# Kernel tuning notes

Hardware: AMD Instinct MI355X
Metric: run time of the kernel (lower is better)

The kernel has to match this reference:

```python
import jax, jax.numpy as jnp
import numpy as np

T, B, N = 12, 2, 1024
M = B * N            # nodes per timestep (batch-flattened)
D_IN, D_H, D_T, D_O = 64, 128, 16, 32


def _linear_params(k, fin, fout):
    kw, kb = jax.random.split(k)
    s = 1.0 / np.sqrt(fin)
    w = jax.random.uniform(kw, (fin, fout), jnp.float32, -s, s)
    b = jax.random.uniform(kb, (fout,), jnp.float32, -s, s)
    return w, b


def setup_inputs() -> dict:
    key = jax.random.key(0)
    ks = jax.random.split(key, 12)
    x = jax.random.normal(ks[0], (T, M, D_IN), jnp.float32)
    A = (jax.random.uniform(ks[1], (T, M, M)) < 0.01).astype(jnp.float32)
    A = A * (1.0 - jnp.eye(M, dtype=jnp.float32))  # no self-loops in raw adjacency
    ego_mask = jax.random.randint(ks[2], (B, T, N), 0, 2).astype(bool)
    gcn1_w, gcn1_b = _linear_params(ks[3], D_IN, D_H)
    gcn2_w, gcn2_b = _linear_params(ks[4], D_H, D_H)
    time_w, time_b = _linear_params(ks[5], 1, D_T)
    q_w, q_b = _linear_params(ks[6], D_H + D_T, D_H)
    k_w, k_b = _linear_params(ks[7], D_H + D_T, D_H)
    v_w, v_b = _linear_params(ks[8], D_H + D_T, D_H)
    o_w, o_b = _linear_params(ks[9], D_H, D_H)
    fc_w, fc_b = _linear_params(ks[10], D_H, D_O)
    return dict(x=x, A=A, ego_mask=ego_mask,
                gcn1_w=gcn1_w, gcn1_b=gcn1_b, gcn2_w=gcn2_w, gcn2_b=gcn2_b,
                time_w=time_w, time_b=time_b,
                q_w=q_w, q_b=q_b, k_w=k_w, k_b=k_b, v_w=v_w, v_b=v_b,
                o_w=o_w, o_b=o_b, fc_w=fc_w, fc_b=fc_b)


def _forward(x, A, ego_mask, gcn1_w, gcn1_b, gcn2_w, gcn2_b, time_w, time_b,
             q_w, q_b, k_w, k_b, v_w, v_b, o_w, o_b, fc_w, fc_b):
    # [B,T,N] -> [T, B*N], as in mask.permute(1,0,2).reshape(T,-1)
    mask = ego_mask.transpose(1, 0, 2).reshape(T, M)
    tvals = jnp.arange(T, dtype=jnp.float32)

    def step(_, inp):
        xt, At, mt, tv = inp  # [M,D_IN], [M,M], [M] bool, scalar
        m = mt.astype(xt.dtype)
        # restrict adjacency to masked subgraph; GCNConv adds self-loops
        A_hat = At * (m[:, None] * m[None, :]) + jnp.diag(m)
        deg = A_hat.sum(axis=0)  # in-degree per target (PyG gcn_norm on col)
        nrm = jnp.where(deg > 0, 1.0 / jnp.sqrt(jnp.maximum(deg, 1e-12)), 0.0)

        def gcn(h, w, b):
            # out[i] = nrm[i] * sum_j A_hat[j,i] * nrm[j] * (hW)[j] + b
            return (A_hat.T @ ((h @ w) * nrm[:, None])) * nrm[:, None] + b

        h = jax.nn.relu(gcn(xt, gcn1_w, gcn1_b))
        h = jax.nn.relu(gcn(h, gcn2_w, gcn2_b))
        # t_vec = sin(Linear(1,D_T)(t)) -- identical for all nodes
        t_vec = jnp.sin(tv * time_w[0] + time_b)  # [D_T]
        xtc = jnp.concatenate([h, jnp.broadcast_to(t_vec, (M, D_T))], axis=-1)
        Q = xtc @ q_w + q_b
        K = xtc @ k_w + k_b
        V = xtc @ v_w + v_b
        scores = (Q @ K.T) * (1.0 / np.sqrt(D_H))  # [M,M]
        scores = jnp.where(mt[None, :], scores, -1e9)  # keys restricted to mask
        agg = jax.nn.softmax(scores, axis=-1) @ V
        out = ((agg @ o_w + o_b) @ fc_w + fc_b) * m[:, None]  # scatter-back == mask
        return None, out

    _, outs = jax.lax.scan(step, None, (x, A, mask, tvals))  # [T,M,D_O]
    return outs.reshape(T, B, N, D_O).transpose(1, 2, 0, 3)  # [B,N,T,D_O]


def reference(x, A, ego_mask, gcn1_w, gcn1_b, gcn2_w, gcn2_b, time_w, time_b,
              q_w, q_b, k_w, k_b, v_w, v_b, o_w, o_b, fc_w, fc_b):
    return _forward(x, A, ego_mask, gcn1_w, gcn1_b, gcn2_w, gcn2_b, time_w,
                    time_b, q_w, q_b, k_w, k_b, v_w, v_b, o_w, o_b, fc_w, fc_b)
```

## Files before the change

kernel.cpp:

```cpp
#include <hip/hip_runtime.h>
#include <stdint.h>

#define TT   12
#define BB   2
#define NN   1024
#define MM   2048
#define TM   24576
#define DIN  64
#define DH   128
#define DOUT 32
#define CAP  64
#define OUTSZ 786432

typedef __attribute__((ext_vector_type(8))) short short8;
typedef __attribute__((ext_vector_type(4))) short short4v;
typedef __attribute__((ext_vector_type(4))) float f32x4;

#define MFMA(a,b,c) __builtin_amdgcn_mfma_f32_16x16x32_bf16((a),(b),(c),0,0,0)

__device__ __forceinline__ float bf2f(unsigned short u){
  union { uint32_t i; float f; } x; x.i = ((uint32_t)u) << 16; return x.f;
}
__device__ __forceinline__ unsigned short f2bf(float f){
  union { float f; uint32_t i; } x; x.f = f;
  uint32_t u = x.i + 0x7FFFu + ((x.i >> 16) & 1u);
  return (unsigned short)(u >> 16);
}
__device__ __forceinline__ float LD(const void* p, size_t i, int mode){
  return mode ? ((const float*)p)[i] : bf2f(((const unsigned short*)p)[i]);
}
__device__ __forceinline__ short8 ldx8(const void* x, size_t off, int md){
  if(md){
    const float4* xf = (const float4*)((const float*)x + off);
    float4 a = xf[0], b = xf[1];
    short8 o;
    o[0]=(short)f2bf(a.x); o[1]=(short)f2bf(a.y); o[2]=(short)f2bf(a.z); o[3]=(short)f2bf(a.w);
    o[4]=(short)f2bf(b.x); o[5]=(short)f2bf(b.y); o[6]=(short)f2bf(b.z); o[7]=(short)f2bf(b.w);
    return o;
  }
  return *(const short8*)((const unsigned short*)x + off);
}

__global__ void k_fill(float* __restrict__ out, int n, float val){
  int i = blockIdx.x*blockDim.x + threadIdx.x;
  if(i < n) out[i] = val;
}

__global__ void k_detect2(const unsigned short* __restrict__ x,
                          const unsigned char* __restrict__ eg,
                          int* __restrict__ dtf, int* __restrict__ flag,
                          int* __restrict__ nact){
  if(blockIdx.x == 0){
    __shared__ int cnt_s;
    if(threadIdx.x==0) cnt_s = 0;
    if(threadIdx.x < TT) nact[threadIdx.x] = 0;
    __syncthreads();
    int c = 0;
    for(int i=threadIdx.x; i<6144; i+=blockDim.x){
      unsigned short h = x[i*2];
      unsigned e = (h >> 7) & 0xFF;
      if(h==0 || (e >= 0x60 && e <= 0x9F)) c++;
    }
    atomicAdd(&cnt_s, c);
    __syncthreads();
    if(threadIdx.x==0) *dtf = (cnt_s > 4000) ? 0 : 1;
  } else {
    __shared__ int pres_s, ge2_s;
    if(threadIdx.x==0){ pres_s=0; ge2_s=0; }
    __syncthreads();
    int pres=0, ge2=0;
    for(int i=threadIdx.x; i<24576; i+=blockDim.x){
      unsigned v = eg[i];
      if(v){ pres |= 1 << (i & 7); if(v >= 2u) ge2 = 1; }
    }
    if(pres) atomicOr(&pres_s, pres);
    if(ge2)  atomicOr(&ge2_s, 1);
    __syncthreads();
    if(threadIdx.x==0){
      int pr = pres_s, g2 = ge2_s, mode;
      if(!g2){
        if((pr & ~0x01) == 0)      mode = 4;
        else if((pr & ~0x11) == 0) mode = 0;
        else                       mode = 1;
      } else {
        if((pr & ~0xC0) == 0)      mode = 5;
        else if((pr & ~0xCC) == 0) mode = 3;
        else                       mode = 2;
      }
      *flag = mode;
    }
  }
}

__global__ void k_mask(const void* __restrict__ egom, const int* __restrict__ flag,
                       int* __restrict__ cnt, int* __restrict__ nact,
                       int* __restrict__ aidx, int* __restrict__ inv,
                       float* __restrict__ out){
  int idx = blockIdx.x*blockDim.x + threadIdx.x;
  out[idx] = 0.f;
  if(idx >= TM) return;
  int t = idx / MM, node = idx % MM;
  int b = node / NN, n = node % NN;
  int src = (b*TT + t)*NN + n;
  int mode = *flag;
  int v;
  if(mode==0)      v = ((const int*)egom)[src] != 0;
  else if(mode==1) v = ((const unsigned char*)egom)[src] != 0;
  else if(mode==2) v = ((const unsigned short*)egom)[src] != 0;
  else if(mode==3) v = ((const float*)egom)[src] != 0.f;
  else if(mode==4) v = ((const long long*)egom)[src] != 0;
  else             v = ((const double*)egom)[src] != 0.0;
  cnt[idx] = 0;
  unsigned long long bal = __ballot(v != 0);
  int lane = threadIdx.x & 63;
  int base = 0;
  if(lane == 0 && bal) base = atomicAdd(&nact[t], __popcll(bal));
  base = __shfl(base, 0, 64);
  int ic = -1;
  if(v){
    int pfx = __popcll(bal & ((1ULL << lane) - 1ULL));
    ic = base + pfx;
    aidx[(size_t)t*MM + ic] = node;
  }
  inv[idx] = ic;
}

__global__ void k_prepw(
  const void* __restrict__ w1, const void* __restrict__ w2,
  const void* __restrict__ qw, const void* __restrict__ kw, const void* __restrict__ vw,
  const void* __restrict__ qb0, const void* __restrict__ kb0, const void* __restrict__ vb0,
  const void* __restrict__ ow, const void* __restrict__ ob,
  const void* __restrict__ fw, const void* __restrict__ fb,
  const void* __restrict__ tw, const void* __restrict__ tb,
  const void* __restrict__ b1, const void* __restrict__ b2,
  const int* __restrict__ dtf,
  unsigned short* __restrict__ W1t, unsigned short* __restrict__ W2t,
  unsigned short* __restrict__ Wqt, unsigned short* __restrict__ Wkt,
  unsigned short* __restrict__ Wvt, unsigned short* __restrict__ Wct,
  float* __restrict__ qbf, float* __restrict__ kbf, float* __restrict__ vbf,
  float* __restrict__ bcf, float* __restrict__ b1f, float* __restrict__ b2f)
{
  const int md = *dtf;
  int id = blockIdx.x*blockDim.x + threadIdx.x;
  if(id < 8192){
    int n=id&127, k2=id>>7; W1t[n*64+k2]=f2bf(LD(w1,(size_t)k2*128+n,md)); return; }
  id -= 8192;
  if(id < 16384){ int n=id&127,k2=id>>7; W2t[n*128+k2]=f2bf(LD(w2,(size_t)k2*128+n,md)); return; }
  id -= 16384;
  if(id < 16384){ int n=id&127,k2=id>>7; Wqt[n*128+k2]=f2bf(LD(qw,(size_t)k2*128+n,md)); return; }
  id -= 16384;
  if(id < 16384){ int n=id&127,k2=id>>7; Wkt[n*128+k2]=f2bf(LD(kw,(size_t)k2*128+n,md)); return; }
  id -= 16384;
  if(id < 16384){ int n=id&127,k2=id>>7; Wvt[n*128+k2]=f2bf(LD(vw,(size_t)k2*128+n,md)); return; }
  id -= 16384;
  if(id < 4096){
    int oc=id&31, c=id>>5; float s=0.f;
    for(int r=0;r<128;r++) s += LD(ow,(size_t)c*128+r,md)*LD(fw,(size_t)r*32+oc,md);
    Wct[oc*128+c]=f2bf(s); return;
  }
  id -= 4096;
  if(id < 32){
    float s = LD(fb,id,md);
    for(int r=0;r<128;r++) s += LD(ob,r,md)*LD(fw,(size_t)r*32+id,md);
    bcf[id]=s; return;
  }
  id -= 32;
  if(id < 4608){
    int which = id/1536, rem=id%1536, t=rem/128, n=rem%128;
    const void* W  = which==0?qw:(which==1?kw:vw);
    const void* Bs = which==0?qb0:(which==1?kb0:vb0);
    float s = LD(Bs,n,md);
    for(int d=0;d<16;d++){
      float tv = sinf((float)t*LD(tw,d,md) + LD(tb,d,md));
      s += tv * LD(W,(size_t)(128+d)*128+n,md);
    }
    float* dst = which==0?qbf:(which==1?kbf:vbf);
    dst[t*128+n]=s; return;
  }
  id -= 4608;
  if(id < 256){
    if(id<128) b1f[id] = LD(b1,id,md);
    else       b2f[id-128] = LD(b2,id-128,md);
    return;
  }
}

__global__ __launch_bounds__(256) void k_edges(const void* __restrict__ A,
    const int* __restrict__ dtf, const int* __restrict__ inv,
    int* __restrict__ cnt, int* __restrict__ edges){
  int id = blockIdx.x*blockDim.x + threadIdx.x;
  int seg = id & 63; int row = id >> 6;
  int t = row / MM;
  int jc = inv[row];
  if(jc < 0) return;
  const int* invt = inv + (size_t)t*MM;
  int* cb = cnt + (size_t)t*MM;
  int* eb = edges + (size_t)t*MM*CAP;
  if(*dtf){
    const float4* p4 = (const float4*)((const float*)A + (size_t)row*MM + seg*32);
    #pragma unroll
    for(int u=0;u<8;u++){
      float4 v = p4[u];
      float wd[4]={v.x,v.y,v.z,v.w};
      #pragma unroll
      for(int q=0;q<4;q++){
        if(wd[q]!=0.f){
          int ibc = invt[seg*32 + u*4 + q];
          if(ibc >= 0){ int s=atomicAdd(&cb[ibc],1); if(s<CAP) eb[(size_t)ibc*CAP+s]=jc; }
        }
      }
    }
  } else {
    const uint4* p4 = (const uint4*)((const unsigned short*)A + (size_t)row*MM + seg*32);
    #pragma unroll
    for(int u=0;u<4;u++){
      uint4 v = p4[u];
      unsigned wd[4]={v.x,v.y,v.z,v.w};
      #pragma unroll
      for(int q=0;q<4;q++){
        int ib = seg*32 + u*8 + q*2;
        if(wd[q] & 0xFFFFu){
          int ibc = invt[ib];
          if(ibc >= 0){ int s=atomicAdd(&cb[ibc],1); if(s<CAP) eb[(size_t)ibc*CAP+s]=jc; }
        }
        if(wd[q] >> 16){
          int ibc = invt[ib+1];
          if(ibc >= 0){ int s=atomicAdd(&cb[ibc],1); if(s<CAP) eb[(size_t)ibc*CAP+s]=jc; }
        }
      }
    }
  }
}

__global__ __launch_bounds__(256) void k_gemm_x(const void* __restrict__ x,
    const int* __restrict__ dtf, const int* __restrict__ nact,
    const int* __restrict__ aidx, const unsigned short* __restrict__ Wt,
    float* __restrict__ g)
{
  const int tile = blockIdx.x*64;
  const int t = tile / MM, il = tile % MM;
  const int na = nact[t];
  if(il >= ((na+63)&~63)) return;
  const int md = *dtf;
  const int tid=threadIdx.x, wv=tid>>6, lane=tid&63, l15=lane&15, quad=lane>>4;
  const int r0 = tile + (wv>>1)*32;
  const int c0 = (wv&1)*64;
  short8 bf[2][4];
  #pragma unroll
  for(int kk=0;kk<2;kk++)
    #pragma unroll
    for(int nt=0;nt<4;nt++)
      bf[kk][nt] = *(const short8*)(Wt + (size_t)(c0+nt*16+l15)*DIN + kk*32 + quad*8);
  const int il0 = (r0 % MM) + l15, il1 = (r0 % MM) + 16 + l15;
  const int n0 = aidx[(size_t)t*MM + (il0 < na ? il0 : 0)];
  const int n1 = aidx[(size_t)t*MM + (il1 < na ? il1 : 0)];
  const size_t xb0 = ((size_t)t*MM + n0)*DIN;
  const size_t xb1 = ((size_t)t*MM + n1)*DIN;
  f32x4 z = {0.f,0.f,0.f,0.f};
  f32x4 acc[2][4];
  #pragma unroll
  for(int i=0;i<2;i++){ acc[i][0]=z; acc[i][1]=z; acc[i][2]=z; acc[i][3]=z; }
  #pragma unroll
  for(int kk=0;kk<2;kk++){
    short8 a0 = ldx8(x, xb0 + kk*32 + quad*8, md);
    short8 a1 = ldx8(x, xb1 + kk*32 + quad*8, md);
    #pragma unroll
    for(int nt=0;nt<4;nt++){
      acc[0][nt]=MFMA(a0,bf[kk][nt],acc[0][nt]);
      acc[1][nt]=MFMA(a1,bf[kk][nt],acc[1][nt]);
    }
  }
  #pragma unroll
  for(int mt=0;mt<2;mt++)
    #pragma unroll
    for(int nt=0;nt<4;nt++){
      int col = c0+nt*16+l15;
      #pragma unroll
      for(int r=0;r<4;r++){
        int row = r0 + mt*16 + quad*4 + r;
        g[(size_t)row*DH + col] = acc[mt][nt][r];
      }
    }
}

__global__ __launch_bounds__(256) void k_gemm_h(const unsigned short* __restrict__ X,
    const unsigned short* __restrict__ Wt, float* __restrict__ g,
    const int* __restrict__ nact)
{
  const int tile = blockIdx.x*64;
  const int t = tile / MM, il = tile % MM;
  const int na = nact[t];
  if(il >= ((na+63)&~63)) return;
  const int tid=threadIdx.x, wv=tid>>6, lane=tid&63, l15=lane&15, quad=lane>>4;
  const int r0 = tile + (wv>>1)*32;
  const int c0 = (wv&1)*64;
  short8 bf[4][4];
  #pragma unroll
  for(int kk=0;kk<4;kk++)
    #pragma unroll
    for(int nt=0;nt<4;nt++)
      bf[kk][nt] = *(const short8*)(Wt + (size_t)(c0+nt*16+l15)*DH + kk*32 + quad*8);
  f32x4 z = {0.f,0.f,0.f,0.f};
  f32x4 acc[2][4];
  #pragma unroll
  for(int i=0;i<2;i++){ acc[i][0]=z; acc[i][1]=z; acc[i][2]=z; acc[i][3]=z; }
  #pragma unroll
  for(int kk=0;kk<4;kk++){
    short8 a0 = *(const short8*)(X + (size_t)(r0+l15)*DH    + kk*32 + quad*8);
    short8 a1 = *(const short8*)(X + (size_t)(r0+16+l15)*DH + kk*32 + quad*8);
    #pragma unroll
    for(int nt=0;nt<4;nt++){
      acc[0][nt]=MFMA(a0,bf[kk][nt],acc[0][nt]);
      acc[1][nt]=MFMA(a1,bf[kk][nt],acc[1][nt]);
    }
  }
  #pragma unroll
  for(int mt=0;mt<2;mt++)
    #pragma unroll
    for(int nt=0;nt<4;nt++){
      int col = c0+nt*16+l15;
      #pragma unroll
      for(int r=0;r<4;r++){
        int row = r0 + mt*16 + quad*4 + r;
        g[(size_t)row*DH + col] = acc[mt][nt][r];
      }
    }
}

__global__ __launch_bounds__(256) void k_gather(const float* __restrict__ g,
    const int* __restrict__ edges, const int* __restrict__ cnt,
    const int* __restrict__ nact, const float* __restrict__ bias,
    unsigned short* __restrict__ h)
{
  int wv = threadIdx.x>>6, lane = threadIdx.x&63;
  int gi = blockIdx.x*4 + wv;
// ... 37 lines not shown
  const int tid=threadIdx.x, wv=tid>>6, lane=tid&63, l15=lane&15, quad=lane>>4;
  const int r0 = tile + (wv>>1)*32;
  const int c0 = (wv&1)*64;
  short8 bf[4][4];
  #pragma unroll
  for(int kk=0;kk<4;kk++)
    #pragma unroll
    for(int nt=0;nt<4;nt++)
      bf[kk][nt] = *(const short8*)(Wt + (size_t)(c0+nt*16+l15)*DH + kk*32 + quad*8);
  f32x4 z = {0.f,0.f,0.f,0.f};
  f32x4 acc[2][4];
  #pragma unroll
  for(int i=0;i<2;i++){ acc[i][0]=z; acc[i][1]=z; acc[i][2]=z; acc[i][3]=z; }
  #pragma unroll
  for(int kk=0;kk<4;kk++){
    short8 a0 = *(const short8*)(X + (size_t)(r0+l15)*DH    + kk*32 + quad*8);
    short8 a1 = *(const short8*)(X + (size_t)(r0+16+l15)*DH + kk*32 + quad*8);
    #pragma unroll
    for(int nt=0;nt<4;nt++){
      acc[0][nt]=MFMA(a0,bf[kk][nt],acc[0][nt]);
      acc[1][nt]=MFMA(a1,bf[kk][nt],acc[1][nt]);
    }
  }
  if(which < 2){
    unsigned short* o = which==0 ? Qo : Ko;
    #pragma unroll
    for(int mt=0;mt<2;mt++)
      #pragma unroll
      for(int nt=0;nt<4;nt++){
        int col = c0+nt*16+l15;
        float bb = bias[t*DH+col];
        #pragma unroll
        for(int r=0;r<4;r++){
          int row = r0 + mt*16 + quad*4 + r;
          o[(size_t)row*DH + col] = f2bf(acc[mt][nt][r] + bb);
        }
      }
  } else {
    #pragma unroll
    for(int mt=0;mt<2;mt++)
      #pragma unroll
      for(int nt=0;nt<4;nt++){
        int col = c0+nt*16+l15;
        float bb = bias[t*DH+col];
        int node0 = il + (wv>>1)*32 + mt*16 + quad*4;
        short4v pk;
        #pragma unroll
        for(int r=0;r<4;r++) pk[r] = (short)f2bf(acc[mt][nt][r] + bb);
        *(short4v*)(Vtc + ((size_t)t*DH + col)*MM + node0) = pk;
      }
  }
}

__global__ __launch_bounds__(256) void k_attn(
  const unsigned short* __restrict__ Q, const unsigned short* __restrict__ Kc,
  const unsigned short* __restrict__ Vtc, const int* __restrict__ nact,
  const int* __restrict__ aidx, const unsigned short* __restrict__ Wct,
  const float* __restrict__ bc, float* __restrict__ out)
{
  __shared__ unsigned short Kl[64][136];
  __shared__ unsigned short Vl[128][72];
  __shared__ short Pl[4][16][72];
  __shared__ short Al[4][16][136];
  const int tid=threadIdx.x, wv=tid>>6, lane=tid&63, l15=lane&15, quad=lane>>4;
  const int t = blockIdx.y;
  const int na = nact[t];
  const int qblk = blockIdx.x*64;
  if(qblk >= na) return;
  const int qbase = qblk + wv*16;
  const float scale = 0.088388347648318447f;
  const int nkt = (na + 63) >> 6;

  short8 bq[4];
  #pragma unroll
  for(int kk=0;kk<4;kk++)
    bq[kk] = *(const short8*)(Q + ((size_t)t*MM + qbase + l15)*DH + kk*32 + quad*8);

  f32x4 zz = {0.f,0.f,0.f,0.f};
  f32x4 accPV[8];
  #pragma unroll
  for(int i=0;i<8;i++) accPV[i]=zz;
  float l_run = 0.f;

  const int srow = tid >> 2, sseg = tid & 3;
  const int vch  = tid >> 1, vhalf = tid & 1;

  short8 kreg[4], vreg[4];
  {
    const unsigned short* gk = Kc + ((size_t)t*MM + srow)*DH + sseg*32;
    const unsigned short* gv = Vtc + ((size_t)t*DH + vch)*MM + vhalf*32;
    #pragma unroll
    for(int j=0;j<4;j++){ kreg[j] = *(const short8*)(gk + j*8);
                          vreg[j] = *(const short8*)(gv + j*8); }
  }

  for(int kt=0; kt<nkt; kt++){
    const int key0 = kt*64;
    __syncthreads();
    {
      short8* kd = (short8*)&Kl[srow][sseg*32];
      short8* vd = (short8*)&Vl[vch][vhalf*32];
      #pragma unroll
      for(int j=0;j<4;j++){ kd[j] = kreg[j]; vd[j] = vreg[j]; }
    }
    __syncthreads();
    if(kt+1 < nkt){
      const int key1 = key0 + 64;
      const unsigned short* gk = Kc + ((size_t)t*MM + key1 + srow)*DH + sseg*32;
      const unsigned short* gv = Vtc + ((size_t)t*DH + vch)*MM + key1 + vhalf*32;
      #pragma unroll
      for(int j=0;j<4;j++){ kreg[j] = *(const short8*)(gk + j*8);
                            vreg[j] = *(const short8*)(gv + j*8); }
    }
    #pragma unroll
    for(int mt=0;mt<4;mt++){
      f32x4 s = zz;
      #pragma unroll
      for(int kk=0;kk<4;kk++){
        short8 ak = *(const short8*)&Kl[mt*16+l15][kk*32 + quad*8];
        s = MFMA(ak, bq[kk], s);
      }
      short4v pk;
      #pragma unroll
      for(int r=0;r<4;r++){
        float sv = fminf(fmaxf(s[r]*scale, -15.f), 15.f);
        float valid = (key0 + mt*16 + quad*4 + r < na) ? 1.f : 0.f;
        float p = __expf(sv) * valid;
        pk[r] = (short)f2bf(p);
        l_run += bf2f((unsigned short)pk[r]);
      }
      *(short4v*)&Pl[wv][l15][mt*16 + quad*4] = pk;
    }
    #pragma unroll
    for(int kk=0;kk<2;kk++){
      short8 ap = *(const short8*)&Pl[wv][l15][kk*32 + quad*8];
      #pragma unroll
      for(int nt=0;nt<8;nt++){
        short8 bv = *(const short8*)&Vl[nt*16+l15][kk*32 + quad*8];
        accPV[nt] = MFMA(ap, bv, accPV[nt]);
      }
    }
  }
  l_run += __shfl_xor(l_run, 16, 64);
  l_run += __shfl_xor(l_run, 32, 64);

  #pragma unroll
  for(int nt=0;nt<8;nt++)
    #pragma unroll
    for(int r=0;r<4;r++){
      float av = fminf(fmaxf(accPV[nt][r], -1e30f), 1e30f);
      Al[wv][quad*4+r][nt*16+l15] = (short)f2bf(av);
    }

  const int qc = qbase + l15;
  const bool qok = (qc < na);
  const float linv = (l_run > 0.f) ? 1.f/l_run : 0.f;
  const int node = aidx[(size_t)t*MM + (qok ? qc : 0)];
  #pragma unroll
  for(int mt2=0;mt2<2;mt2++){
    f32x4 d = zz;
    #pragma unroll
    for(int kk=0;kk<4;kk++){
      short8 aw = *(const short8*)(Wct + (size_t)(mt2*16+l15)*DH + kk*32 + quad*8);
      short8 bl = *(const short8*)&Al[wv][l15][kk*32 + quad*8];
      d = MFMA(aw, bl, d);
    }
    f32x4 bcv = *(const f32x4*)(bc + mt2*16 + quad*4);
    f32x4 o4;
    #pragma unroll
    for(int r=0;r<4;r++) o4[r] = d[r]*linv + bcv[r];
    if(qok)
      *(f32x4*)(out + (size_t)node*(TT*DOUT) + (size_t)t*DOUT + mt2*16 + quad*4) = o4;
  }
}

extern "C" void kernel_launch(void* const* d_in, const int* in_sizes, int n_in,
                              void* d_out, int out_size, void* d_ws, size_t ws_size,
                              hipStream_t stream)
{
  float* outp = (float*)d_out;
  static const int EXP[19] = {1572864,50331648,24576,8192,128,16384,128,16,16,
                              18432,128,18432,128,18432,128,16384,128,4096,32};
  bool ok = (n_in >= 19) && (out_size == OUTSZ);
  if(ok) for(int i=0;i<19;i++) if(in_sizes[i] != EXP[i]) { ok = false; break; }
  if(!ok){
    k_fill<<<(out_size+255)/256,256,0,stream>>>(outp, out_size, 1000.f);
    return;
  }
  const void* x   = d_in[0];
  const void* A   = d_in[1];
  const void* eg  = d_in[2];
  const void* w1  = d_in[3];
  const void* b1  = d_in[4];
  const void* w2  = d_in[5];
  const void* b2  = d_in[6];
  const void* tw  = d_in[7];
  const void* tb  = d_in[8];
  const void* qw  = d_in[9];
  const void* qb0 = d_in[10];
  const void* kw  = d_in[11];
  const void* kb0 = d_in[12];
  const void* vw  = d_in[13];
  const void* vb0 = d_in[14];
  const void* ow  = d_in[15];
  const void* ob  = d_in[16];
  const void* fw  = d_in[17];
  const void* fb  = d_in[18];

  char* w = (char*)d_ws;
  size_t off = 0;
  auto alloc = [&](size_t sz)->char*{
    char* p = w + off; off = (off + sz + 255) & ~(size_t)255; return p; };
  int*   flag  = (int*)  alloc(4);
  int*   dtf   = (int*)  alloc(4);
  int*   nactb = (int*)  alloc(TT*4);
  int*   cnt   = (int*)  alloc((size_t)TM*4);
  int*   aidx  = (int*)  alloc((size_t)TM*4);
  int*   inv   = (int*)  alloc((size_t)TM*4);
  int*   edges = (int*)  alloc((size_t)TM*CAP*4);
  float* g     = (float*)alloc((size_t)TM*DH*4);
  unsigned short* h   = (unsigned short*)alloc((size_t)TM*DH*2);
  unsigned short* Vtc = (unsigned short*)alloc((size_t)TT*DH*MM*2);
  unsigned short* W1t = (unsigned short*)alloc(DH*DIN*2);
  unsigned short* W2t = (unsigned short*)alloc(DH*DH*2);
  unsigned short* Wqt = (unsigned short*)alloc(DH*DH*2);
  unsigned short* Wkt = (unsigned short*)alloc(DH*DH*2);
  unsigned short* Wvt = (unsigned short*)alloc(DH*DH*2);
  unsigned short* Wct = (unsigned short*)alloc(DOUT*DH*2);
  float* qbf = (float*)alloc(TT*DH*4);
  float* kbf = (float*)alloc(TT*DH*4);
  float* vbf = (float*)alloc(TT*DH*4);
  float* bcf = (float*)alloc(DOUT*4);
  float* b1f = (float*)alloc(DH*4);
  float* b2f = (float*)alloc(DH*4);
  if(off > ws_size){
    k_fill<<<(out_size+255)/256,256,0,stream>>>(outp, out_size, 500.f);
    return;
  }

  unsigned short* Qb = (unsigned short*)g;
  unsigned short* Kb = (unsigned short*)((char*)g + (size_t)TM*DH*2);

  k_detect2<<<2,256,0,stream>>>((const unsigned short*)x, (const unsigned char*)eg,
                                dtf, flag, nactb);
  k_mask<<<OUTSZ/256,256,0,stream>>>(eg, flag, cnt, nactb, aidx, inv, outp);
  k_prepw<<<(82720+255)/256,256,0,stream>>>(w1,w2,qw,kw,vw,qb0,kb0,vb0,ow,ob,fw,fb,tw,tb,
                                            b1,b2,dtf,
                                            W1t,W2t,Wqt,Wkt,Wvt,Wct,qbf,kbf,vbf,bcf,b1f,b2f);
  k_edges<<<TM*64/256,256,0,stream>>>(A, dtf, inv, cnt, edges);
  k_gemm_x<<<TM/64,256,0,stream>>>(x, dtf, nactb, aidx, W1t, g);
  k_gather<<<TM/4,256,0,stream>>>(g, edges, cnt, nactb, b1f, h);
  k_gemm_h<<<TM/64,256,0,stream>>>(h, W2t, g, nactb);
  k_gather<<<TM/4,256,0,stream>>>(g, edges, cnt, nactb, b2f, h);
  k_gemm_qkv<<<dim3(TM/64,1,3),256,0,stream>>>(h, Wqt,Wkt,Wvt, qbf,kbf,vbf, Qb,Kb,Vtc, nactb);
  k_attn<<<dim3(MM/64,TT),256,0,stream>>>(Qb, Kb, Vtc, nactb, aidx, Wct, bcf, outp);
}
```

Measured before the change: 517.3 us.

## Split attention over key chunks and merge prep with edge building

The attention kernel is split along the key dimension into KS=4 partitions (split-K style). Each partition writes unnormalized PV accumulators and row sums to a workspace, and a finalize kernel sums them and applies the fused output projection. Because scores are clamped and no running max is used, partials can be added directly. Weight preparation and edge construction are also fused into one launch, saving a kernel launch. The main aim is more blocks for attention, which previously had only about 32x12 blocks with about half active per timestep. The cost is extra global traffic for the partial accumulators (~50MB fp32) and one extra launch.

```diff
diff --git a/kernel.cpp b/kernel.cpp
--- a/kernel.cpp
+++ b/kernel.cpp
@@ -11,6 +11,8 @@
 #define DOUT 32
 #define CAP  64
 #define OUTSZ 786432
+#define KS   4
+#define PWB  324
 
 typedef __attribute__((ext_vector_type(8))) short short8;
 typedef __attribute__((ext_vector_type(4))) short short4v;
@@ -125,7 +127,7 @@
   inv[idx] = ic;
 }
 
-__global__ void k_prepw(
+__global__ __launch_bounds__(256) void k_prep_edges(
   const void* __restrict__ w1, const void* __restrict__ w2,
   const void* __restrict__ qw, const void* __restrict__ kw, const void* __restrict__ vw,
   const void* __restrict__ qb0, const void* __restrict__ kb0, const void* __restrict__ vb0,
@@ -138,94 +140,94 @@
   unsigned short* __restrict__ Wqt, unsigned short* __restrict__ Wkt,
   unsigned short* __restrict__ Wvt, unsigned short* __restrict__ Wct,
   float* __restrict__ qbf, float* __restrict__ kbf, float* __restrict__ vbf,
-  float* __restrict__ bcf, float* __restrict__ b1f, float* __restrict__ b2f)
+  float* __restrict__ bcf, float* __restrict__ b1f, float* __restrict__ b2f,
+  const void* __restrict__ A, const int* __restrict__ inv,
+  int* __restrict__ cnt, int* __restrict__ edges)
 {
   const int md = *dtf;
-  int id = blockIdx.x*blockDim.x + threadIdx.x;
-  if(id < 8192){
-    int n=id&127, k2=id>>7; W1t[n*64+k2]=f2bf(LD(w1,(size_t)k2*128+n,md)); return; }
-  id -= 8192;
-  if(id < 16384){ int n=id&127,k2=id>>7; W2t[n*128+k2]=f2bf(LD(w2,(size_t)k2*128+n,md)); return; }
-  id -= 16384;
-  if(id < 16384){ int n=id&127,k2=id>>7; Wqt[n*128+k2]=f2bf(LD(qw,(size_t)k2*128+n,md)); return; }
-  id -= 16384;
-  if(id < 16384){ int n=id&127,k2=id>>7; Wkt[n*128+k2]=f2bf(LD(kw,(size_t)k2*128+n,md)); return; }
-  id -= 16384;
-  if(id < 16384){ int n=id&127,k2=id>>7; Wvt[n*128+k2]=f2bf(LD(vw,(size_t)k2*128+n,md)); return; }
-  id -= 16384;
-  if(id < 4096){
-    int oc=id&31, c=id>>5; float s=0.f;
-    for(int r=0;r<128;r++) s += LD(ow,(size_t)c*128+r,md)*LD(fw,(size_t)r*32+oc,md);
-    Wct[oc*128+c]=f2bf(s); return;
-  }
-  id -= 4096;
-  if(id < 32){
-    float s = LD(fb,id,md);
-    for(int r=0;r<128;r++) s += LD(ob,r,md)*LD(fw,(size_t)r*32+id,md);
-    bcf[id]=s; return;
-  }
-  id -= 32;
-  if(id < 4608){
-    int which = id/1536, rem=id%1536, t=rem/128, n=rem%128;
-    const void* W  = which==0?qw:(which==1?kw:vw);
-    const void* Bs = which==0?qb0:(which==1?kb0:vb0);
-    float s = LD(Bs,n,md);
-    for(int d=0;d<16;d++){
-      float tv = sinf((float)t*LD(tw,d,md) + LD(tb,d,md));
-      s += tv * LD(W,(size_t)(128+d)*128+n,md);
-    }
-    float* dst = which==0?qbf:(which==1?kbf:vbf);
-    dst[t*128+n]=s; return;
-  }
-  id -= 4608;
-  if(id < 256){
-    if(id<128) b1f[id] = LD(b1,id,md);
-    else       b2f[id-128] = LD(b2,id-128,md);
-    return;
-  }
-}
-
-__global__ __launch_bounds__(256) void k_edges(const void* __restrict__ A,
-    const int* __restrict__ dtf, const int* __restrict__ inv,
-    int* __restrict__ cnt, int* __restrict__ edges){
-  int id = blockIdx.x*blockDim.x + threadIdx.x;
-  int seg = id & 63; int row = id >> 6;
-  int t = row / MM;
-  int jc = inv[row];
-  if(jc < 0) return;
-  const int* invt = inv + (size_t)t*MM;
-  int* cb = cnt + (size_t)t*MM;
-  int* eb = edges + (size_t)t*MM*CAP;
-  if(*dtf){
-    const float4* p4 = (const float4*)((const float*)A + (size_t)row*MM + seg*32);
-    #pragma unroll
-    for(int u=0;u<8;u++){
-      float4 v = p4[u];
-      float wd[4]={v.x,v.y,v.z,v.w};
-      #pragma unroll
-      for(int q=0;q<4;q++){
-        if(wd[q]!=0.f){
-          int ibc = invt[seg*32 + u*4 + q];
-          if(ibc >= 0){ int s=atomicAdd(&cb[ibc],1); if(s<CAP) eb[(size_t)ibc*CAP+s]=jc; }
+  if(blockIdx.x < PWB){
+    int id = blockIdx.x*blockDim.x + threadIdx.x;
+    if(id < 8192){
+      int n=id&127, k2=id>>7; W1t[n*64+k2]=f2bf(LD(w1,(size_t)k2*128+n,md)); return; }
+    id -= 8192;
+    if(id < 16384){ int n=id&127,k2=id>>7; W2t[n*128+k2]=f2bf(LD(w2,(size_t)k2*128+n,md)); return; }
+    id -= 16384;
+    if(id < 16384){ int n=id&127,k2=id>>7; Wqt[n*128+k2]=f2bf(LD(qw,(size_t)k2*128+n,md)); return; }
+    id -= 16384;
+    if(id < 16384){ int n=id&127,k2=id>>7; Wkt[n*128+k2]=f2bf(LD(kw,(size_t)k2*128+n,md)); return; }
+    id -= 16384;
+    if(id < 16384){ int n=id&127,k2=id>>7; Wvt[n*128+k2]=f2bf(LD(vw,(size_t)k2*128+n,md)); return; }
+    id -= 16384;
+    if(id < 4096){
+      int oc=id&31, c=id>>5; float s=0.f;
+      for(int r=0;r<128;r++) s += LD(ow,(size_t)c*128+r,md)*LD(fw,(size_t)r*32+oc,md);
+      Wct[oc*128+c]=f2bf(s); return;
+    }
+    id -= 4096;
+    if(id < 32){
+      float s = LD(fb,id,md);
+      for(int r=0;r<128;r++) s += LD(ob,r,md)*LD(fw,(size_t)r*32+id,md);
+      bcf[id]=s; return;
+    }
+    id -= 32;
+    if(id < 4608){
+      int which = id/1536, rem=id%1536, t=rem/128, n=rem%128;
+      const void* W  = which==0?qw:(which==1?kw:vw);
+      const void* Bs = which==0?qb0:(which==1?kb0:vb0);
+      float s = LD(Bs,n,md);
+      for(int d=0;d<16;d++){
+        float tv = sinf((float)t*LD(tw,d,md) + LD(tb,d,md));
+        s += tv * LD(W,(size_t)(128+d)*128+n,md);
+      }
+      float* dst = which==0?qbf:(which==1?kbf:vbf);
+      dst[t*128+n]=s; return;
+    }
+    id -= 4608;
+    if(id < 256){
+      if(id<128) b1f[id] = LD(b1,id,md);
+      else       b2f[id-128] = LD(b2,id-128,md);
+      return;
+    }
+  } else {
+    int id = (blockIdx.x - PWB)*blockDim.x + threadIdx.x;
+    int seg = id & 63; int row = id >> 6;
+    int t = row / MM;
+    int jc = inv[row];
+    if(jc < 0) return;
+    const int* invt = inv + (size_t)t*MM;
+    int* cb = cnt + (size_t)t*MM;
+    int* eb = edges + (size_t)t*MM*CAP;
+    if(md){
+      const float4* p4 = (const float4*)((const float*)A + (size_t)row*MM + seg*32);
+      #pragma unroll
+      for(int u=0;u<8;u++){
+        float4 v = p4[u];
+        float wd[4]={v.x,v.y,v.z,v.w};
+        #pragma unroll
+        for(int q=0;q<4;q++){
+          if(wd[q]!=0.f){
+            int ibc = invt[seg*32 + u*4 + q];
+            if(ibc >= 0){ int s=atomicAdd(&cb[ibc],1); if(s<CAP) eb[(size_t)ibc*CAP+s]=jc; }
+          }
         }
       }
-    }
-  } else {
-    const uint4* p4 = (const uint4*)((const unsigned short*)A + (size_t)row*MM + seg*32);
-    #pragma unroll
-    for(int u=0;u<4;u++){
-      uint4 v = p4[u];
-      unsigned wd[4]={v.x,v.y,v.z,v.w};
-      #pragma unroll
-      for(int q=0;q<4;q++){
-        int ib = seg*32 + u*8 + q*2;
-        if(wd[q] & 0xFFFFu){
-          int ibc = invt[ib];
-          if(ibc >= 0){ int s=atomicAdd(&cb[ibc],1); if(s<CAP) eb[(size_t)ibc*CAP+s]=jc; }
-        }
-        if(wd[q] >> 16){
-          int ibc = invt[ib+1];
-          if(ibc >= 0){ int s=atomicAdd(&cb[ibc],1); if(s<CAP) eb[(size_t)ibc*CAP+s]=jc; }
+    } else {
+      const uint4* p4 = (const uint4*)((const unsigned short*)A + (size_t)row*MM + seg*32);
+      #pragma unroll
+      for(int u=0;u<4;u++){
+        uint4 v = p4[u];
+        unsigned wd[4]={v.x,v.y,v.z,v.w};
+        #pragma unroll
+        for(int q=0;q<4;q++){
+          int ib = seg*32 + u*8 + q*2;
+          if(wd[q] & 0xFFFFu){
+            int ibc = invt[ib];
+            if(ibc >= 0){ int s=atomicAdd(&cb[ibc],1); if(s<CAP) eb[(size_t)ibc*CAP+s]=jc; }
+          }
+          if(wd[q] >> 16){
+            int ibc = invt[ib+1];
+            if(ibc >= 0){ int s=atomicAdd(&cb[ibc],1); if(s<CAP) eb[(size_t)ibc*CAP+s]=jc; }
+          }
         }
       }
     }
@@ -424,15 +426,105 @@
   }
 }
 
-__global__ __launch_bounds__(256) void k_attn(
+__global__ __launch_bounds__(256) void k_attn_part(
   const unsigned short* __restrict__ Q, const unsigned short* __restrict__ Kc,
   const unsigned short* __restrict__ Vtc, const int* __restrict__ nact,
-  const int* __restrict__ aidx, const unsigned short* __restrict__ Wct,
-  const float* __restrict__ bc, float* __restrict__ out)
+  float* __restrict__ pacc, float* __restrict__ plr)
 {
   __shared__ unsigned short Kl[64][136];
   __shared__ unsigned short Vl[128][72];
   __shared__ short Pl[4][16][72];
+  const int tid=threadIdx.x, wv=tid>>6, lane=tid&63, l15=lane&15, quad=lane>>4;
+  const int t = blockIdx.y, s = blockIdx.z;
+  const int na = nact[t];
+  const int qblk = blockIdx.x*64;
+  if(qblk >= na) return;
+  const int qbase = qblk + wv*16;
+  const float scale = 0.088388347648318447f;
+  const int nkt = (na + 63) >> 6;
+
+  short8 bq[4];
+  #pragma unroll
+  for(int kk=0;kk<4;kk++)
+    bq[kk] = *(const short8*)(Q + ((size_t)t*MM + qbase + l15)*DH + kk*32 + quad*8);
+
+  f32x4 zz = {0.f,0.f,0.f,0.f};
+  f32x4 accPV[8];
+  #pragma unroll
+  for(int i=0;i<8;i++) accPV[i]=zz;
+  float l_run = 0.f;
+
+  const int srow = tid >> 2, sseg = tid & 3;
+  const int vch  = tid >> 1, vhalf = tid & 1;
+
+  short8 kreg[4], vreg[4];
+  if(s < nkt){
+    const unsigned short* gk = Kc + ((size_t)t*MM + s*64 + srow)*DH + sseg*32;
+    const unsigned short* gv = Vtc + ((size_t)t*DH + vch)*MM + s*64 + vhalf*32;
+    #pragma unroll
+    for(int j=0;j<4;j++){ kreg[j] = *(const short8*)(gk + j*8);
+                          vreg[j] = *(const short8*)(gv + j*8); }
+  }
+
+  for(int kt=s; kt<nkt; kt+=KS){
+    const int key0 = kt*64;
+    __syncthreads();
+    {
+      short8* kd = (short8*)&Kl[srow][sseg*32];
+      short8* vd = (short8*)&Vl[vch][vhalf*32];
+      #pragma unroll
+      for(int j=0;j<4;j++){ kd[j] = kreg[j]; vd[j] = vreg[j]; }
+    }
+    __syncthreads();
+    if(kt+KS < nkt){
+      const int key1 = key0 + KS*64;
+      const unsigned short* gk = Kc + ((size_t)t*MM + key1 + srow)*DH + sseg*32;
+      const unsigned short* gv = Vtc + ((size_t)t*DH + vch)*MM + key1 + vhalf*32;
+      #pragma unroll
+      for(int j=0;j<4;j++){ kreg[j] = *(const short8*)(gk + j*8);
+                            vreg[j] = *(const short8*)(gv + j*8); }
+    }
+    #pragma unroll
+    for(int mt=0;mt<4;mt++){
+      f32x4 sv4 = zz;
+      #pragma unroll
+      for(int kk=0;kk<4;kk++){
+        short8 ak = *(const short8*)&Kl[mt*16+l15][kk*32 + quad*8];
+        sv4 = MFMA(ak, bq[kk], sv4);
+      }
+      short4v pk;
+      #pragma unroll
+      for(int r=0;r<4;r++){
+        float sv = fminf(fmaxf(sv4[r]*scale, -15.f), 15.f);
+        float valid = (key0 + mt*16 + quad*4 + r < na) ? 1.f : 0.f;
+        float p = __expf(sv) * valid;
+        pk[r] = (short)f2bf(p);
+        l_run += bf2f((unsigned short)pk[r]);
+      }
+      *(short4v*)&Pl[wv][l15][mt*16 + quad*4] = pk;
+    }
+    #pragma unroll
+    for(int kk=0;kk<2;kk++){
+      short8 ap = *(const short8*)&Pl[wv][l15][kk*32 + quad*8];
+      #pragma unroll
+      for(int nt=0;nt<8;nt++){
+        short8 bv = *(const short8*)&Vl[nt*16+l15][kk*32 + quad*8];
+        accPV[nt] = MFMA(ap, bv, accPV[nt]);
+      }
+    }
+  }
+  float* pb = pacc + ((((size_t)s*TT + t)*32 + blockIdx.x)*256 + tid)*32;
+  #pragma unroll
+  for(int i=0;i<8;i++) *(f32x4*)(pb + i*4) = accPV[i];
+  plr[(((size_t)s*TT + t)*32 + blockIdx.x)*256 + tid] = l_run;
+}
+
+__global__ __launch_bounds__(256) void k_attn_fin(
+  const float* __restrict__ pacc, const float* __restrict__ plr,
+  const int* __restrict__ nact, const int* __restrict__ aidx,
+  const unsigned short* __restrict__ Wct, const float* __restrict__ bc,
+  float* __restrict__ out)
+{
   __shared__ short Al[4][16][136];
   const int tid=threadIdx.x, wv=tid>>6, lane=tid&63, l15=lane&15, quad=lane>>4;
   const int t = blockIdx.y;
@@ -440,78 +532,18 @@
   const int qblk = blockIdx.x*64;
   if(qblk >= na) return;
   const int qbase = qblk + wv*16;
-  const float scale = 0.088388347648318447f;
-  const int nkt = (na + 63) >> 6;
-
-  short8 bq[4];
-  #pragma unroll
-  for(int kk=0;kk<4;kk++)
-    bq[kk] = *(const short8*)(Q + ((size_t)t*MM + qbase + l15)*DH + kk*32 + quad*8);
 
   f32x4 zz = {0.f,0.f,0.f,0.f};
-  f32x4 accPV[8];
-  #pragma unroll
-  for(int i=0;i<8;i++) accPV[i]=zz;
+  f32x4 acc[8];
+  #pragma unroll
+  for(int i=0;i<8;i++) acc[i]=zz;
   float l_run = 0.f;
-
-  const int srow = tid >> 2, sseg = tid & 3;
-  const int vch  = tid >> 1, vhalf = tid & 1;
-
-  short8 kreg[4], vreg[4];
-  {
-    const unsigned short* gk = Kc + ((size_t)t*MM + srow)*DH + sseg*32;
-    const unsigned short* gv = Vtc + ((size_t)t*DH + vch)*MM + vhalf*32;
-    #pragma unroll
-    for(int j=0;j<4;j++){ kreg[j] = *(const short8*)(gk + j*8);
-                          vreg[j] = *(const short8*)(gv + j*8); }
-  }
-
-  for(int kt=0; kt<nkt; kt++){
-    const int key0 = kt*64;
-    __syncthreads();
-    {
-      short8* kd = (short8*)&Kl[srow][sseg*32];
-      short8* vd = (short8*)&Vl[vch][vhalf*32];
-      #pragma unroll
-      for(int j=0;j<4;j++){ kd[j] = kreg[j]; vd[j] = vreg[j]; }
-    }
-    __syncthreads();
-    if(kt+1 < nkt){
-      const int key1 = key0 + 64;
-      const unsigned short* gk = Kc + ((size_t)t*MM + key1 + srow)*DH + sseg*32;
-      const unsigned short* gv = Vtc + ((size_t)t*DH + vch)*MM + key1 + vhalf*32;
-      #pragma unroll
-      for(int j=0;j<4;j++){ kreg[j] = *(const short8*)(gk + j*8);
-                            vreg[j] = *(const short8*)(gv + j*8); }
-    }
-    #pragma unroll
-    for(int mt=0;mt<4;mt++){
-      f32x4 s = zz;
-      #pragma unroll
-      for(int kk=0;kk<4;kk++){
-        short8 ak = *(const short8*)&Kl[mt*16+l15][kk*32 + quad*8];
-        s = MFMA(ak, bq[kk], s);
-      }
-      short4v pk;
-      #pragma unroll
-      for(int r=0;r<4;r++){
-        float sv = fminf(fmaxf(s[r]*scale, -15.f), 15.f);
-        float valid = (key0 + mt*16 + quad*4 + r < na) ? 1.f : 0.f;
-        float p = __expf(sv) * valid;
-        pk[r] = (short)f2bf(p);
-        l_run += bf2f((unsigned short)pk[r]);
-      }
-      *(short4v*)&Pl[wv][l15][mt*16 + quad*4] = pk;
-    }
-    #pragma unroll
-    for(int kk=0;kk<2;kk++){
-      short8 ap = *(const short8*)&Pl[wv][l15][kk*32 + quad*8];
-      #pragma unroll
-      for(int nt=0;nt<8;nt++){
-        short8 bv = *(const short8*)&Vl[nt*16+l15][kk*32 + quad*8];
-        accPV[nt] = MFMA(ap, bv, accPV[nt]);
-      }
-    }
+  #pragma unroll
+  for(int s=0;s<KS;s++){
+    const f32x4* p = (const f32x4*)(pacc + ((((size_t)s*TT + t)*32 + blockIdx.x)*256 + tid)*32);
+    #pragma unroll
+    for(int i=0;i<8;i++) acc[i] += p[i];
+    l_run += plr[(((size_t)s*TT + t)*32 + blockIdx.x)*256 + tid];
   }
   l_run += __shfl_xor(l_run, 16, 64);
   l_run += __shfl_xor(l_run, 32, 64);
@@ -520,7 +552,7 @@
   for(int nt=0;nt<8;nt++)
     #pragma unroll
     for(int r=0;r<4;r++){
-      float av = fminf(fmaxf(accPV[nt][r], -1e30f), 1e30f);
+      float av = fminf(fmaxf(acc[nt][r], -1e30f), 1e30f);
       Al[wv][quad*4+r][nt*16+l15] = (short)f2bf(av);
     }
 
@@ -605,6 +637,8 @@
   float* bcf = (float*)alloc(DOUT*4);
   float* b1f = (float*)alloc(DH*4);
   float* b2f = (float*)alloc(DH*4);
+  float* pacc = (float*)alloc((size_t)KS*TT*32*256*32*4);
+  float* plr  = (float*)alloc((size_t)KS*TT*32*256*4);
   if(off > ws_size){
     k_fill<<<(out_size+255)/256,256,0,stream>>>(outp, out_size, 500.f);
     return;
@@ -616,14 +650,15 @@
   k_detect2<<<2,256,0,stream>>>((const unsigned short*)x, (const unsigned char*)eg,
                                 dtf, flag, nactb);
   k_mask<<<OUTSZ/256,256,0,stream>>>(eg, flag, cnt, nactb, aidx, inv, outp);
-  k_prepw<<<(82720+255)/256,256,0,stream>>>(w1,w2,qw,kw,vw,qb0,kb0,vb0,ow,ob,fw,fb,tw,tb,
-                                            b1,b2,dtf,
-                                            W1t,W2t,Wqt,Wkt,Wvt,Wct,qbf,kbf,vbf,bcf,b1f,b2f);
-  k_edges<<<TM*64/256,256,0,stream>>>(A, dtf, inv, cnt, edges);
+  k_prep_edges<<<PWB + TM*64/256,256,0,stream>>>(w1,w2,qw,kw,vw,qb0,kb0,vb0,ow,ob,fw,fb,tw,tb,
+                                                 b1,b2,dtf,
+                                                 W1t,W2t,Wqt,Wkt,Wvt,Wct,qbf,kbf,vbf,bcf,b1f,b2f,
+                                                 A, inv, cnt, edges);
   k_gemm_x<<<TM/64,256,0,stream>>>(x, dtf, nactb, aidx, W1t, g);
   k_gather<<<TM/4,256,0,stream>>>(g, edges, cnt, nactb, b1f, h);
   k_gemm_h<<<TM/64,256,0,stream>>>(h, W2t, g, nactb);
   k_gather<<<TM/4,256,0,stream>>>(g, edges, cnt, nactb, b2f, h);
   k_gemm_qkv<<<dim3(TM/64,1,3),256,0,stream>>>(h, Wqt,Wkt,Wvt, qbf,kbf,vbf, Qb,Kb,Vtc, nactb);
-  k_attn<<<dim3(MM/64,TT),256,0,stream>>>(Qb, Kb, Vtc, nactb, aidx, Wct, bcf, outp);
-}
+  k_attn_part<<<dim3(MM/64,TT,KS),256,0,stream>>>(Qb, Kb, Vtc, nactb, pacc, plr);
+  k_attn_fin<<<dim3(MM/64,TT),256,0,stream>>>(pacc, plr, nactb, aidx, Wct, bcf, outp);
+}
```

Result: no change. 507.9 us (-1.8%).

## Fuse detection, masking, weight prep, edge building and first GEMM into fewer launches

Applied to the files above, without the earlier changes.

Merges the dtype-detection and mask-compaction kernels into one kernel that gives each timestep its own block and computes the compaction order deterministically. Weight prep, edge extraction and the first GCN GEMM now share a single launch, split by block index, and each block recomputes the float-format detection locally. The first GEMM reads and converts W1 directly instead of using a pre-transposed copy. This removes several launches and serialization points. In exchange every block in the fused kernel repeats the x-scan detection, and mask compaction now runs on only twelve blocks.

```diff
diff --git a/kernel.cpp b/kernel.cpp
--- a/kernel.cpp
+++ b/kernel.cpp
@@ -11,6 +11,7 @@
 #define DOUT 32
 #define CAP  64
 #define OUTSZ 786432
+#define PWB  292
 
 typedef __attribute__((ext_vector_type(8))) short short8;
 typedef __attribute__((ext_vector_type(4))) short short4v;
@@ -46,105 +47,88 @@
   if(i < n) out[i] = val;
 }
 
-__global__ void k_detect2(const unsigned short* __restrict__ x,
-                          const unsigned char* __restrict__ eg,
-                          int* __restrict__ dtf, int* __restrict__ flag,
-                          int* __restrict__ nact){
-  if(blockIdx.x == 0){
-    __shared__ int cnt_s;
-    if(threadIdx.x==0) cnt_s = 0;
-    if(threadIdx.x < TT) nact[threadIdx.x] = 0;
-    __syncthreads();
-    int c = 0;
-    for(int i=threadIdx.x; i<6144; i+=blockDim.x){
-      unsigned short h = x[i*2];
-      unsigned e = (h >> 7) & 0xFF;
-      if(h==0 || (e >= 0x60 && e <= 0x9F)) c++;
-    }
-    atomicAdd(&cnt_s, c);
-    __syncthreads();
-    if(threadIdx.x==0) *dtf = (cnt_s > 4000) ? 0 : 1;
-  } else {
-    __shared__ int pres_s, ge2_s;
-    if(threadIdx.x==0){ pres_s=0; ge2_s=0; }
-    __syncthreads();
-    int pres=0, ge2=0;
-    for(int i=threadIdx.x; i<24576; i+=blockDim.x){
-      unsigned v = eg[i];
+__global__ __launch_bounds__(256) void k_maskdet(
+    const void* __restrict__ egom,
+    int* __restrict__ cnt, int* __restrict__ nact,
+    int* __restrict__ aidx, int* __restrict__ inv,
+    float* __restrict__ out)
+{
+  const int bid = blockIdx.x, tid = threadIdx.x;
+  out[(size_t)bid*256 + tid] = 0.f;
+  if(bid >= TT) return;
+  const int t = bid, lane = tid & 63, wv = tid >> 6;
+
+  __shared__ int pres_s, ge2_s, wcnt_s[4];
+  if(tid == 0){ pres_s = 0; ge2_s = 0; }
+  __syncthreads();
+  {
+    int pres = 0, ge2 = 0;
+    const unsigned char* egp = (const unsigned char*)egom;
+    for(int i = tid; i < 24576; i += 256){
+      unsigned v = egp[i];
       if(v){ pres |= 1 << (i & 7); if(v >= 2u) ge2 = 1; }
     }
     if(pres) atomicOr(&pres_s, pres);
     if(ge2)  atomicOr(&ge2_s, 1);
+  }
+  __syncthreads();
+  int mode;
+  {
+    int pr = pres_s, g2 = ge2_s;
+    if(!g2){
+      if((pr & ~0x01) == 0)      mode = 4;
+      else if((pr & ~0x11) == 0) mode = 0;
+      else                       mode = 1;
+    } else {
+      if((pr & ~0xC0) == 0)      mode = 5;
+      else if((pr & ~0xCC) == 0) mode = 3;
+      else                       mode = 2;
+    }
+  }
+
+  int base = 0;
+  for(int r = 0; r < 8; r++){
+    int node = r*256 + tid;
+    int b = node / NN, n = node % NN;
+    int src = (b*TT + t)*NN + n;
+    int v;
+    if(mode==0)      v = ((const int*)egom)[src] != 0;
+    else if(mode==1) v = ((const unsigned char*)egom)[src] != 0;
+    else if(mode==2) v = ((const unsigned short*)egom)[src] != 0;
+    else if(mode==3) v = ((const float*)egom)[src] != 0.f;
+    else if(mode==4) v = ((const long long*)egom)[src] != 0;
+    else             v = ((const double*)egom)[src] != 0.0;
+    cnt[(size_t)t*MM + node] = 0;
+    unsigned long long bal = __ballot(v != 0);
+    if(lane == 0) wcnt_s[wv] = __popcll(bal);
     __syncthreads();
-    if(threadIdx.x==0){
-      int pr = pres_s, g2 = ge2_s, mode;
-      if(!g2){
-        if((pr & ~0x01) == 0)      mode = 4;
-        else if((pr & ~0x11) == 0) mode = 0;
-        else                       mode = 1;
-      } else {
-        if((pr & ~0xC0) == 0)      mode = 5;
-        else if((pr & ~0xCC) == 0) mode = 3;
-        else                       mode = 2;
-      }
-      *flag = mode;
-    }
-  }
-}
-
-__global__ void k_mask(const void* __restrict__ egom, const int* __restrict__ flag,
-                       int* __restrict__ cnt, int* __restrict__ nact,
-                       int* __restrict__ aidx, int* __restrict__ inv,
-                       float* __restrict__ out){
-  int idx = blockIdx.x*blockDim.x + threadIdx.x;
-  out[idx] = 0.f;
-  if(idx >= TM) return;
-  int t = idx / MM, node = idx % MM;
-  int b = node / NN, n = node % NN;
-  int src = (b*TT + t)*NN + n;
-  int mode = *flag;
-  int v;
-  if(mode==0)      v = ((const int*)egom)[src] != 0;
-  else if(mode==1) v = ((const unsigned char*)egom)[src] != 0;
-  else if(mode==2) v = ((const unsigned short*)egom)[src] != 0;
-  else if(mode==3) v = ((const float*)egom)[src] != 0.f;
-  else if(mode==4) v = ((const long long*)egom)[src] != 0;
-  else             v = ((const double*)egom)[src] != 0.0;
-  cnt[idx] = 0;
-  unsigned long long bal = __ballot(v != 0);
-  int lane = threadIdx.x & 63;
-  int base = 0;
-  if(lane == 0 && bal) base = atomicAdd(&nact[t], __popcll(bal));
-  base = __shfl(base, 0, 64);
-  int ic = -1;
-  if(v){
-    int pfx = __popcll(bal & ((1ULL << lane) - 1ULL));
-    ic = base + pfx;
-    aidx[(size_t)t*MM + ic] = node;
-  }
-  inv[idx] = ic;
-}
-
-__global__ void k_prepw(
-  const void* __restrict__ w1, const void* __restrict__ w2,
-  const void* __restrict__ qw, const void* __restrict__ kw, const void* __restrict__ vw,
-  const void* __restrict__ qb0, const void* __restrict__ kb0, const void* __restrict__ vb0,
-  const void* __restrict__ ow, const void* __restrict__ ob,
-  const void* __restrict__ fw, const void* __restrict__ fb,
-  const void* __restrict__ tw, const void* __restrict__ tb,
-  const void* __restrict__ b1, const void* __restrict__ b2,
-  const int* __restrict__ dtf,
-  unsigned short* __restrict__ W1t, unsigned short* __restrict__ W2t,
-  unsigned short* __restrict__ Wqt, unsigned short* __restrict__ Wkt,
-  unsigned short* __restrict__ Wvt, unsigned short* __restrict__ Wct,
-  float* __restrict__ qbf, float* __restrict__ kbf, float* __restrict__ vbf,
-  float* __restrict__ bcf, float* __restrict__ b1f, float* __restrict__ b2f)
-{
-  const int md = *dtf;
-  int id = blockIdx.x*blockDim.x + threadIdx.x;
-  if(id < 8192){
-    int n=id&127, k2=id>>7; W1t[n*64+k2]=f2bf(LD(w1,(size_t)k2*128+n,md)); return; }
-  id -= 8192;
+    int mybase = base;
+    for(int w2 = 0; w2 < wv; w2++) mybase += wcnt_s[w2];
+    int ic = -1;
+    if(v){
+      ic = mybase + __popcll(bal & ((1ULL << lane) - 1ULL));
+      aidx[(size_t)t*MM + ic] = node;
+    }
+    inv[(size_t)t*MM + node] = ic;
+    base += wcnt_s[0] + wcnt_s[1] + wcnt_s[2] + wcnt_s[3];
+    __syncthreads();
+  }
+  if(tid == 0) nact[t] = base;
+}
+
+
+__device__ __forceinline__ void dev_prepw2_item(int id, int md,
+  const void* w2,
+  const void* qw, const void* kw, const void* vw,
+  const void* qb0, const void* kb0, const void* vb0,
+  const void* ow, const void* ob, const void* fw, const void* fb,
+  const void* tw, const void* tb, const void* b1, const void* b2,
+  unsigned short* W2t,
+  unsigned short* Wqt, unsigned short* Wkt,
+  unsigned short* Wvt, unsigned short* Wct,
+  float* qbf, float* kbf, float* vbf,
+  float* bcf, float* b1f, float* b2f)
+{
   if(id < 16384){ int n=id&127,k2=id>>7; W2t[n*128+k2]=f2bf(LD(w2,(size_t)k2*128+n,md)); return; }
   id -= 16384;
   if(id < 16384){ int n=id&127,k2=id>>7; Wqt[n*128+k2]=f2bf(LD(qw,(size_t)k2*128+n,md)); return; }
@@ -185,10 +169,8 @@
   }
 }
 
-__global__ __launch_bounds__(256) void k_edges(const void* __restrict__ A,
-    const int* __restrict__ dtf, const int* __restrict__ inv,
-    int* __restrict__ cnt, int* __restrict__ edges){
-  int id = blockIdx.x*blockDim.x + threadIdx.x;
+__device__ __forceinline__ void dev_edges_item(int id, int md,
+    const void* A, const int* inv, int* cnt, int* edges){
   int seg = id & 63; int row = id >> 6;
   int t = row / MM;
   int jc = inv[row];
@@ -196,7 +178,7 @@
   const int* invt = inv + (size_t)t*MM;
   int* cb = cnt + (size_t)t*MM;
   int* eb = edges + (size_t)t*MM*CAP;
-  if(*dtf){
+  if(md){
     const float4* p4 = (const float4*)((const float*)A + (size_t)row*MM + seg*32);
     #pragma unroll
     for(int u=0;u<8;u++){
@@ -232,25 +214,29 @@
   }
 }
 
-__global__ __launch_bounds__(256) void k_gemm_x(const void* __restrict__ x,
-    const int* __restrict__ dtf, const int* __restrict__ nact,
-    const int* __restrict__ aidx, const unsigned short* __restrict__ Wt,
-    float* __restrict__ g)
-{
-  const int tile = blockIdx.x*64;
+__device__ __forceinline__ void dev_gemm_x_direct(int tileIdx, int md, int tid,
+    const void* x, const int* nact, const int* aidx,
+    const void* w1, float* g)
+{
+  const int tile = tileIdx*64;
   const int t = tile / MM, il = tile % MM;
   const int na = nact[t];
   if(il >= ((na+63)&~63)) return;
-  const int md = *dtf;
-  const int tid=threadIdx.x, wv=tid>>6, lane=tid&63, l15=lane&15, quad=lane>>4;
+  const int wv=tid>>6, lane=tid&63, l15=lane&15, quad=lane>>4;
   const int r0 = tile + (wv>>1)*32;
   const int c0 = (wv&1)*64;
   short8 bf[2][4];
   #pragma unroll
   for(int kk=0;kk<2;kk++)
     #pragma unroll
-    for(int nt=0;nt<4;nt++)
-      bf[kk][nt] = *(const short8*)(Wt + (size_t)(c0+nt*16+l15)*DIN + kk*32 + quad*8);
+    for(int nt=0;nt<4;nt++){
+      const int col = c0+nt*16+l15;
+      short8 o;
+      #pragma unroll
+      for(int j=0;j<8;j++)
+        o[j] = (short)f2bf(LD(w1, (size_t)(kk*32 + quad*8 + j)*DH + col, md));
+      bf[kk][nt] = o;
+    }
   const int il0 = (r0 % MM) + l15, il1 = (r0 % MM) + 16 + l15;
   const int n0 = aidx[(size_t)t*MM + (il0 < na ? il0 : 0)];
   const int n1 = aidx[(size_t)t*MM + (il1 < na ? il1 : 0)];
@@ -281,6 +267,51 @@
         g[(size_t)row*DH + col] = acc[mt][nt][r];
       }
     }
+}
+
+__global__ __launch_bounds__(256) void k_pex(
+  const void* __restrict__ x, const void* __restrict__ A,
+  const void* __restrict__ w1, const void* __restrict__ w2,
+  const void* __restrict__ qw, const void* __restrict__ kw, const void* __restrict__ vw,
+  const void* __restrict__ qb0, const void* __restrict__ kb0, const void* __restrict__ vb0,
+  const void* __restrict__ ow, const void* __restrict__ ob,
+  const void* __restrict__ fw, const void* __restrict__ fb,
+  const void* __restrict__ tw, const void* __restrict__ tb,
+  const void* __restrict__ b1, const void* __restrict__ b2,
+  const int* __restrict__ inv, int* __restrict__ cnt, int* __restrict__ edges,
+  const int* __restrict__ nact, const int* __restrict__ aidx, float* __restrict__ g,
+  unsigned short* __restrict__ W2t,
+  unsigned short* __restrict__ Wqt, unsigned short* __restrict__ Wkt,
+  unsigned short* __restrict__ Wvt, unsigned short* __restrict__ Wct,
+  float* __restrict__ qbf, float* __restrict__ kbf, float* __restrict__ vbf,
+  float* __restrict__ bcf, float* __restrict__ b1f, float* __restrict__ b2f)
+{
+  const int tid = threadIdx.x;
+  __shared__ int cnt_s;
+  if(tid == 0) cnt_s = 0;
+  __syncthreads();
+  {
+    int c = 0;
+    const unsigned short* xs = (const unsigned short*)x;
+    for(int i = tid; i < 6144; i += 256){
+      unsigned short hh = xs[i*2];
+      unsigned e = (hh >> 7) & 0xFF;
+      if(hh==0 || (e >= 0x60 && e <= 0x9F)) c++;
+    }
+    if(c) atomicAdd(&cnt_s, c);
+  }
+  __syncthreads();
+  const int md = (cnt_s > 4000) ? 0 : 1;
+
+  const int b = blockIdx.x;
+  if(b < PWB){
+    dev_prepw2_item(b*256 + tid, md, w2, qw,kw,vw, qb0,kb0,vb0, ow,ob,fw,fb, tw,tb, b1,b2,
+                    W2t, Wqt, Wkt, Wvt, Wct, qbf, kbf, vbf, bcf, b1f, b2f);
+  } else if(b < PWB + TM*64/256){
+    dev_edges_item((b - PWB)*256 + tid, md, A, inv, cnt, edges);
+  } else {
+    dev_gemm_x_direct(b - PWB - TM*64/256, md, tid, x, nact, aidx, w1, g);
+  }
 }
 
 __global__ __launch_bounds__(256) void k_gemm_h(const unsigned short* __restrict__ X,
@@ -545,6 +576,7 @@
       *(f32x4*)(out + (size_t)node*(TT*DOUT) + (size_t)t*DOUT + mt2*16 + quad*4) = o4;
   }
 }
+
 
 extern "C" void kernel_launch(void* const* d_in, const int* in_sizes, int n_in,
                               void* d_out, int out_size, void* d_ws, size_t ws_size,
@@ -583,8 +615,6 @@
   size_t off = 0;
   auto alloc = [&](size_t sz)->char*{
     char* p = w + off; off = (off + sz + 255) & ~(size_t)255; return p; };
-  int*   flag  = (int*)  alloc(4);
-  int*   dtf   = (int*)  alloc(4);
   int*   nactb = (int*)  alloc(TT*4);
   int*   cnt   = (int*)  alloc((size_t)TM*4);
   int*   aidx  = (int*)  alloc((size_t)TM*4);
@@ -593,7 +623,6 @@
   float* g     = (float*)alloc((size_t)TM*DH*4);
   unsigned short* h   = (unsigned short*)alloc((size_t)TM*DH*2);
   unsigned short* Vtc = (unsigned short*)alloc((size_t)TT*DH*MM*2);
-  unsigned short* W1t = (unsigned short*)alloc(DH*DIN*2);
   unsigned short* W2t = (unsigned short*)alloc(DH*DH*2);
   unsigned short* Wqt = (unsigned short*)alloc(DH*DH*2);
   unsigned short* Wkt = (unsigned short*)alloc(DH*DH*2);
@@ -613,14 +642,11 @@
   unsigned short* Qb = (unsigned short*)g;
   unsigned short* Kb = (unsigned short*)((char*)g + (size_t)TM*DH*2);
 
-  k_detect2<<<2,256,0,stream>>>((const unsigned short*)x, (const unsigned char*)eg,
-                                dtf, flag, nactb);
-  k_mask<<<OUTSZ/256,256,0,stream>>>(eg, flag, cnt, nactb, aidx, inv, outp);
-  k_prepw<<<(82720+255)/256,256,0,stream>>>(w1,w2,qw,kw,vw,qb0,kb0,vb0,ow,ob,fw,fb,tw,tb,
-                                            b1,b2,dtf,
-                                            W1t,W2t,Wqt,Wkt,Wvt,Wct,qbf,kbf,vbf,bcf,b1f,b2f);
-  k_edges<<<TM*64/256,256,0,stream>>>(A, dtf, inv, cnt, edges);
-  k_gemm_x<<<TM/64,256,0,stream>>>(x, dtf, nactb, aidx, W1t, g);
+  k_maskdet<<<OUTSZ/256,256,0,stream>>>(eg, cnt, nactb, aidx, inv, outp);
+  k_pex<<<PWB + TM*64/256 + TM/64,256,0,stream>>>(
+      x, A, w1, w2, qw, kw, vw, qb0, kb0, vb0, ow, ob, fw, fb, tw, tb, b1, b2,
+      inv, cnt, edges, nactb, aidx, g,
+      W2t, Wqt, Wkt, Wvt, Wct, qbf, kbf, vbf, bcf, b1f, b2f);
   k_gather<<<TM/4,256,0,stream>>>(g, edges, cnt, nactb, b1f, h);
   k_gemm_h<<<TM/64,256,0,stream>>>(h, W2t, g, nactb);
   k_gather<<<TM/4,256,0,stream>>>(g, edges, cnt, nactb, b2f, h);
```

After: 491.5 us. 5.0% less time.
